# Kernel optimization log

Hardware: AMD Instinct MI355X
Metric: run time of the kernel (lower is better)

## Reference

```python
import jax, jax.numpy as jnp
import numpy as np

HEADS = 8
WS = 8  # window_size


def _relative_position_index(ws):
    coords = np.stack(np.meshgrid(np.arange(ws), np.arange(ws), indexing='ij')).reshape(2, -1)
    rel = coords[:, :, None] - coords[:, None, :]          # [2, N, N]
    rel = rel.transpose(1, 2, 0).copy()                     # [N, N, 2]
    rel[:, :, 0] += ws - 1
    rel[:, :, 1] += ws - 1
    rel[:, :, 0] *= 2 * ws - 1
    return rel.sum(-1)                                      # [N, N] int


def _window_partition(x, ws):
    B, C, H, W = x.shape
    x = x.reshape(B, C, H // ws, ws, W // ws, ws)
    x = jnp.transpose(x, (0, 2, 4, 1, 3, 5))
    return x.reshape(-1, C, ws, ws)


def _window_reverse(windows, ws, H, W):
    C = windows.shape[1]
    B = windows.shape[0] // ((H // ws) * (W // ws))
    x = windows.reshape(B, H // ws, W // ws, C, ws, ws)
    x = jnp.transpose(x, (0, 3, 1, 4, 2, 5))
    return x.reshape(B, C, H, W)


def setup_inputs() -> dict:
    key = jax.random.key(0)
    k1, k2, k3, k4 = jax.random.split(key, 4)
    B, C, H, W = 8, 256, 128, 128
    q = jax.random.normal(k1, (B, C, H, W), dtype=jnp.float32)
    k = jax.random.normal(k2, (B, C, H, W), dtype=jnp.float32)
    v = jax.random.normal(k3, (B, C, H, W), dtype=jnp.float32)
    bias_table = jax.random.normal(k4, ((2 * WS - 1) ** 2, HEADS), dtype=jnp.float32) * 0.02
    return {"q": q, "k": k, "v": v, "bias_table": bias_table, "shift_size": 4}


def reference(q, k, v, bias_table, shift_size):
    B, C, H, W = q.shape
    N = WS * WS
    hd = C // HEADS
    if shift_size > 0:
        q = jnp.roll(q, shift=(-shift_size, -shift_size), axis=(2, 3))
    qw = _window_partition(q, WS)   # [B_, C, ws, ws]
    kw = _window_partition(k, WS)
    vw = _window_partition(v, WS)
    B_ = qw.shape[0]
    # [B_, heads, hd, N] -> q,v as [B_, heads, N, hd]
    qh = jnp.transpose(qw.reshape(B_, HEADS, hd, N), (0, 1, 3, 2))
    kh = kw.reshape(B_, HEADS, hd, N)
    vh = jnp.transpose(vw.reshape(B_, HEADS, hd, N), (0, 1, 3, 2))
    scale = 1.0 / (hd ** 0.5)
    attn = jnp.einsum('bhnd,bhdm->bhnm', qh, kh) * scale
    rel_idx = _relative_position_index(WS)                  # [N, N]
    bias = bias_table[rel_idx.reshape(-1)].reshape(N, N, HEADS)
    bias = jnp.transpose(bias, (2, 0, 1))                   # [heads, N, N]
    attn = jax.nn.softmax(attn + bias[None], axis=-1)
    out = jnp.einsum('bhnm,bhmd->bhnd', attn, vh)           # [B_, heads, N, hd]
    out = jnp.transpose(out, (0, 1, 3, 2)).reshape(B_, C, WS, WS)
    x = _window_reverse(out, WS, H, W)
    if shift_size > 0:
        x = jnp.roll(x, shift=(shift_size, shift_size), axis=(2, 3))
    return x
```

## Files before the change

kernel.cpp:

```cpp
#include <hip/hip_runtime.h>


typedef __attribute__((ext_vector_type(8))) _Float16 half8;
typedef __attribute__((ext_vector_type(2))) __fp16 fp16x2;
typedef __attribute__((ext_vector_type(4))) float f32x4;
typedef unsigned int u32;

#define WSZ 8
#define HGT 128
#define WID 128
#define HWSZ (HGT * WID)
#define CCH 256
#define NHEADS 8
#define HDIM 32
#define VP 72

union __attribute__((aligned(16))) WaveBuf {
  struct { _Float16 k[32 * 72]; _Float16 q[32 * 72]; } kq;
  struct { _Float16 v[32 * VP + 8]; float o[64 * 17]; } vo;
};

__device__ __forceinline__ void lds_fence() {
  asm volatile("s_waitcnt lgkmcnt(0)" ::: "memory");
}
__device__ __forceinline__ u32 h2u(fp16x2 h) {
  union { fp16x2 h; u32 u; } c; c.h = h; return c.u;
}

__global__ void __launch_bounds__(256, 4) wattn_kernel(
    const float* __restrict__ qg, const float* __restrict__ kg,
    const float* __restrict__ vg, const float* __restrict__ btg,
    const int* __restrict__ shiftp, float* __restrict__ outg) {

  __shared__ WaveBuf wb[4];
  __shared__ float bias_lds[226];

  const int tid  = threadIdx.x;
  const int wave = tid >> 6;
  const int lane = tid & 63;
  const int quad = lane >> 4;
  const int c16  = lane & 15;

  const int bid  = blockIdx.x;
  const int wg   = bid & 3;
  const int wh   = (bid >> 2) & 15;
  const int th   = bid >> 6;
  const int head = th & (NHEADS - 1);
  const int b    = th >> 3;
  const int ww   = wg * 4 + wave;

  const int sh   = *shiftp;
  const int base = (b * CCH + head * HDIM) * HWSZ;

  f32x4 vf[8];
  {
    const float* vb = vg + base + (wh * WSZ) * WID + wg * 32;
#pragma unroll
    for (int i = 0; i < 8; ++i) {
      const int flat = i * 256 + tid;
      const int col4 = flat & 7;
      const int row  = (flat >> 3) & 7;
      const int ch   = flat >> 6;
      vf[i] = *(const f32x4*)(vb + ch * HWSZ + row * WID + col4 * 4);
    }
  }

  for (int t = tid; t < 225; t += 256)
    bias_lds[t] = btg[t * NHEADS + head] * 1.44269504088896f;

  {
    const float* kb_g = kg + base + (wh * WSZ) * WID + wg * 32;
#pragma unroll
    for (int i = 0; i < 8; ++i) {
      const int flat = i * 256 + tid;
      const int col4 = flat & 7;
      const int row  = (flat >> 3) & 7;
      const int ch   = flat >> 6;
      const f32x4 f = *(const f32x4*)(kb_g + ch * HWSZ + row * WID + col4 * 4);
      const int w  = col4 >> 1;
      const int un = (2 * row + (col4 & 1)) ^ (((ch >> 3) << 2) | (ch & 3));
      uint2 u;
      u.x = h2u(__builtin_amdgcn_cvt_pkrtz(f.x, f.y));
      u.y = h2u(__builtin_amdgcn_cvt_pkrtz(f.z, f.w));
      *(uint2*)&wb[w].kq.k[ch * 72 + un * 4] = u;
    }
  }

  if ((sh & 3) == 0) {
#pragma unroll
    for (int i = 0; i < 8; ++i) {
      const int flat = i * 256 + tid;
      const int col4 = flat & 7;
      const int row  = (flat >> 3) & 7;
      const int ch   = flat >> 6;
      const int grow = (wh * WSZ + row + sh) & (HGT - 1);
      const int gc0  = (wg * 32 + col4 * 4 + sh) & (WID - 1);
      const f32x4 f = *(const f32x4*)(qg + base + ch * HWSZ + grow * WID + gc0);
      const int w  = col4 >> 1;
      const int un = (2 * row + (col4 & 1)) ^ (((ch >> 3) << 2) | (ch & 3));
      uint2 u;
      u.x = h2u(__builtin_amdgcn_cvt_pkrtz(f.x, f.y));
      u.y = h2u(__builtin_amdgcn_cvt_pkrtz(f.z, f.w));
      *(uint2*)&wb[w].kq.q[ch * 72 + un * 4] = u;
    }
  } else {
#pragma unroll
    for (int i = 0; i < 8; ++i) {
      const int flat = i * 256 + tid;
      const int col4 = flat & 7;
      const int row  = (flat >> 3) & 7;
      const int ch   = flat >> 6;
      const int grow = (wh * WSZ + row + sh) & (HGT - 1);
      const float* qrow = qg + base + ch * HWSZ + grow * WID;
      const int cb = wg * 32 + col4 * 4 + sh;
      const float x0 = qrow[(cb + 0) & (WID - 1)];
      const float x1 = qrow[(cb + 1) & (WID - 1)];
      const float x2 = qrow[(cb + 2) & (WID - 1)];
      const float x3 = qrow[(cb + 3) & (WID - 1)];
      const int w  = col4 >> 1;
      const int un = (2 * row + (col4 & 1)) ^ (((ch >> 3) << 2) | (ch & 3));
      uint2 u;
      u.x = h2u(__builtin_amdgcn_cvt_pkrtz(x0, x1));
      u.y = h2u(__builtin_amdgcn_cvt_pkrtz(x2, x3));
      *(uint2*)&wb[w].kq.q[ch * 72 + un * 4] = u;
    }
  }

  uint2 vu[8];
#pragma unroll
  for (int i = 0; i < 8; ++i) {
    vu[i].x = h2u(__builtin_amdgcn_cvt_pkrtz(vf[i].x, vf[i].y));
    vu[i].y = h2u(__builtin_amdgcn_cvt_pkrtz(vf[i].z, vf[i].w));
  }

  __syncthreads();

  half8 aK[4], bQ[4];
  {
    const _Float16* kb = wb[wave].kq.k;
    const _Float16* qb = wb[wave].kq.q;
#pragma unroll
    for (int j = 0; j < 8; ++j) {
      const int ch = quad * 8 + j;
      const int P  = (quad << 2) | (j & 3);
      const int rb = ch * 72 + (c16 & 3);
#pragma unroll
      for (int t = 0; t < 4; ++t) {
        const int un = ((t * 4 + (c16 >> 2)) ^ P) * 4;
        aK[t][j] = kb[rb + un];
        bQ[t][j] = qb[rb + un];
      }
    }
  }

  const f32x4 zero4 = {0.f, 0.f, 0.f, 0.f};
  const float scale2 = 0.17677669529663687f * 1.44269504088896f;

  int tsub[4];
#pragma unroll
  for (int reg = 0; reg < 4; ++reg) {
    const int t = quad * 4 + reg;
    tsub[reg] = (t >> 3) * 15 + (t & 7);
  }

  u32 pk01[4][4], pk23[4][4];
  float rinv[4];

#pragma unroll
  for (int tc = 0; tc < 4; ++tc) {
    f32x4 sc[4];
#pragma unroll
    for (int tr = 0; tr < 4; ++tr)
      sc[tr] = __builtin_amdgcn_mfma_f32_16x16x32_f16(aK[tr], bQ[tc], zero4, 0, 0, 0);
    const int q64 = tc * 16 + c16;
    const int qb  = ((q64 >> 3) + 7) * 15 + (q64 & 7) + 7;
    float e[4][4], s = 0.f;
#pragma unroll
    for (int tr = 0; tr < 4; ++tr)
#pragma unroll
      for (int reg = 0; reg < 4; ++reg) {
        const float ev = __builtin_amdgcn_exp2f(
            fmaf(sc[tr][reg], scale2, bias_lds[qb - tr * 30 - tsub[reg]]));
        e[tr][reg] = ev; s += ev;
      }
    s += __shfl_xor(s, 16); s += __shfl_xor(s, 32);
    rinv[tc] = __builtin_amdgcn_rcpf(s);
#pragma unroll
    for (int tr = 0; tr < 4; ++tr) {
      pk01[tr][tc] = h2u(__builtin_amdgcn_cvt_pkrtz(e[tr][0], e[tr][1]));
      pk23[tr][tc] = h2u(__builtin_amdgcn_cvt_pkrtz(e[tr][2], e[tr][3]));
    }
  }

  __syncthreads();

  {
#pragma unroll
    for (int i = 0; i < 8; ++i) {
      const int flat = i * 256 + tid;
      const int col4 = flat & 7;
      const int row  = (flat >> 3) & 7;
      const int ch   = flat >> 6;
      const int w  = col4 >> 1;
      const int kb = row * 8 + (col4 & 1) * 4;
      *(uint2*)&wb[w].vo.v[ch * VP + kb] = vu[i];
    }
  }

  __syncthreads();

  half8 aV[2][2];
#pragma unroll
  for (int mt = 0; mt < 2; ++mt)
#pragma unroll
    for (int kc = 0; kc < 2; ++kc)
      aV[mt][kc] = *(const half8*)&wb[wave].vo.v[(mt * 16 + c16) * VP + kc * 32 + quad * 8];

  const int s0 = ((lane & 16) << 1) | c16;
  const int s1 = s0 + 16;
  const bool hi = (lane & 32) != 0;

  f32x4 of2[2][4];
#pragma unroll
  for (int mt = 0; mt < 2; ++mt)
#pragma unroll
    for (int nt = 0; nt < 4; ++nt) of2[mt][nt] = zero4;

#pragma unroll
  for (int nt = 0; nt < 4; ++nt)
#pragma unroll
    for (int kc = 0; kc < 2; ++kc) {
      const int t0 = kc * 2, t1 = kc * 2 + 1;
      const u32 w0a = __shfl(pk01[t0][nt], s0), w0b = __shfl(pk01[t1][nt], s0);
      const u32 w1a = __shfl(pk23[t0][nt], s0), w1b = __shfl(pk23[t1][nt], s0);
      const u32 w2a = __shfl(pk01[t0][nt], s1), w2b = __shfl(pk01[t1][nt], s1);
      const u32 w3a = __shfl(pk23[t0][nt], s1), w3b = __shfl(pk23[t1][nt], s1);
      union { u32 u[4]; half8 h; } bp;
      bp.u[0] = hi ? w0b : w0a;
      bp.u[1] = hi ? w1b : w1a;
      bp.u[2] = hi ? w2b : w2a;
      bp.u[3] = hi ? w3b : w3a;
#pragma unroll
      for (int mt = 0; mt < 2; ++mt)
        of2[mt][nt] = __builtin_amdgcn_mfma_f32_16x16x32_f16(aV[mt][kc], bp.h,
                                                             of2[mt][nt], 0, 0, 0);
    }

  const int hq = (wh * WSZ + (lane >> 3) + sh) & (HGT - 1);
  const int wq = (ww * WSZ + (lane & 7) + sh) & (WID - 1);
  float* ob = outg + base + hq * WID + wq;
  float* obuf = wb[wave].vo.o;

#pragma unroll
  for (int mt = 0; mt < 2; ++mt) {
    lds_fence();
#pragma unroll
    for (int nt = 0; nt < 4; ++nt)
#pragma unroll
      for (int reg = 0; reg < 4; ++reg)
        obuf[(nt * 16 + c16) * 17 + quad * 4 + reg] = of2[mt][nt][reg] * rinv[nt];
    lds_fence();
#pragma unroll
    for (int c = 0; c < 16; ++c)
      ob[(mt * 16 + c) * HWSZ] = obuf[lane * 17 + c];
  }
}

extern "C" void kernel_launch(void* const* d_in, const int* in_sizes, int n_in,
                              void* d_out, int out_size, void* d_ws, size_t ws_size,
                              hipStream_t stream) {
  const float* q  = (const float*)d_in[0];
  const float* k  = (const float*)d_in[1];
  const float* v  = (const float*)d_in[2];
  const float* bt = (const float*)d_in[3];
  const int*   sh = (const int*)d_in[4];
  float* out = (float*)d_out;

  dim3 grid(4096), block(256);
  hipLaunchKernelGGL(wattn_kernel, grid, block, 0, stream, q, k, v, bt, sh, out);
}
```

Measured before the change: 442.1 us.

## Make blocks persistent over four window groups and prefetch next K/Q

Each block now handles four consecutive column groups of windows in a loop, so the grid shrinks by four. The K and Q global loads for the next group are issued into registers before the current group's output store, so memory latency overlaps with compute and writes. Per-block bias setup is amortised across the four groups. In exchange there are fewer blocks to hide latency, more register pressure from the prefetch buffers, and an extra barrier per iteration.

```diff
diff --git a/kernel.cpp b/kernel.cpp
--- a/kernel.cpp
+++ b/kernel.cpp
@@ -27,6 +27,42 @@
   union { fp16x2 h; u32 u; } c; c.h = h; return c.u;
 }
 
+__device__ __forceinline__ void issue_kq(
+    const float* __restrict__ kg, const float* __restrict__ qg,
+    int base, int wh, int wg, int sh, int tid, f32x4* kf, f32x4* qf) {
+  const float* kb_g = kg + base + (wh * WSZ) * WID + wg * 32;
+#pragma unroll
+  for (int i = 0; i < 8; ++i) {
+    const int flat = i * 256 + tid;
+    const int col4 = flat & 7, row = (flat >> 3) & 7, ch = flat >> 6;
+    kf[i] = *(const f32x4*)(kb_g + ch * HWSZ + row * WID + col4 * 4);
+  }
+  if ((sh & 3) == 0) {
+#pragma unroll
+    for (int i = 0; i < 8; ++i) {
+      const int flat = i * 256 + tid;
+      const int col4 = flat & 7, row = (flat >> 3) & 7, ch = flat >> 6;
+      const int grow = (wh * WSZ + row + sh) & (HGT - 1);
+      const int gc0  = (wg * 32 + col4 * 4 + sh) & (WID - 1);
+      qf[i] = *(const f32x4*)(qg + base + ch * HWSZ + grow * WID + gc0);
+    }
+  } else {
+#pragma unroll
+    for (int i = 0; i < 8; ++i) {
+      const int flat = i * 256 + tid;
+      const int col4 = flat & 7, row = (flat >> 3) & 7, ch = flat >> 6;
+      const int grow = (wh * WSZ + row + sh) & (HGT - 1);
+      const float* qrow = qg + base + ch * HWSZ + grow * WID;
+      const int cb = wg * 32 + col4 * 4 + sh;
+      qf[i].x = qrow[(cb + 0) & (WID - 1)];
+      qf[i].y = qrow[(cb + 1) & (WID - 1)];
+      qf[i].z = qrow[(cb + 2) & (WID - 1)];
+      qf[i].w = qrow[(cb + 3) & (WID - 1)];
+    }
+  }
+  __builtin_amdgcn_sched_barrier(0);
+}
+
 __global__ void __launch_bounds__(256, 4) wattn_kernel(
     const float* __restrict__ qg, const float* __restrict__ kg,
     const float* __restrict__ vg, const float* __restrict__ btg,
@@ -42,119 +78,16 @@
   const int c16  = lane & 15;
 
   const int bid  = blockIdx.x;
-  const int wg   = bid & 3;
-  const int wh   = (bid >> 2) & 15;
-  const int th   = bid >> 6;
+  const int wh   = bid & 15;
+  const int th   = bid >> 4;
   const int head = th & (NHEADS - 1);
   const int b    = th >> 3;
-  const int ww   = wg * 4 + wave;
 
   const int sh   = *shiftp;
   const int base = (b * CCH + head * HDIM) * HWSZ;
 
-  f32x4 vf[8];
-  {
-    const float* vb = vg + base + (wh * WSZ) * WID + wg * 32;
-#pragma unroll
-    for (int i = 0; i < 8; ++i) {
-      const int flat = i * 256 + tid;
-      const int col4 = flat & 7;
-      const int row  = (flat >> 3) & 7;
-      const int ch   = flat >> 6;
-      vf[i] = *(const f32x4*)(vb + ch * HWSZ + row * WID + col4 * 4);
-    }
-  }
-
   for (int t = tid; t < 225; t += 256)
     bias_lds[t] = btg[t * NHEADS + head] * 1.44269504088896f;
-
-  {
-    const float* kb_g = kg + base + (wh * WSZ) * WID + wg * 32;
-#pragma unroll
-    for (int i = 0; i < 8; ++i) {
-      const int flat = i * 256 + tid;
-      const int col4 = flat & 7;
-      const int row  = (flat >> 3) & 7;
-      const int ch   = flat >> 6;
-      const f32x4 f = *(const f32x4*)(kb_g + ch * HWSZ + row * WID + col4 * 4);
-      const int w  = col4 >> 1;
-      const int un = (2 * row + (col4 & 1)) ^ (((ch >> 3) << 2) | (ch & 3));
-      uint2 u;
-      u.x = h2u(__builtin_amdgcn_cvt_pkrtz(f.x, f.y));
-      u.y = h2u(__builtin_amdgcn_cvt_pkrtz(f.z, f.w));
-      *(uint2*)&wb[w].kq.k[ch * 72 + un * 4] = u;
-    }
-  }
-
-  if ((sh & 3) == 0) {
-#pragma unroll
-    for (int i = 0; i < 8; ++i) {
-      const int flat = i * 256 + tid;
-      const int col4 = flat & 7;
-      const int row  = (flat >> 3) & 7;
-      const int ch   = flat >> 6;
-      const int grow = (wh * WSZ + row + sh) & (HGT - 1);
-      const int gc0  = (wg * 32 + col4 * 4 + sh) & (WID - 1);
-      const f32x4 f = *(const f32x4*)(qg + base + ch * HWSZ + grow * WID + gc0);
-      const int w  = col4 >> 1;
-      const int un = (2 * row + (col4 & 1)) ^ (((ch >> 3) << 2) | (ch & 3));
-      uint2 u;
-      u.x = h2u(__builtin_amdgcn_cvt_pkrtz(f.x, f.y));
-      u.y = h2u(__builtin_amdgcn_cvt_pkrtz(f.z, f.w));
-      *(uint2*)&wb[w].kq.q[ch * 72 + un * 4] = u;
-    }
-  } else {
-#pragma unroll
-    for (int i = 0; i < 8; ++i) {
-      const int flat = i * 256 + tid;
-      const int col4 = flat & 7;
-      const int row  = (flat >> 3) & 7;
-      const int ch   = flat >> 6;
-      const int grow = (wh * WSZ + row + sh) & (HGT - 1);
-      const float* qrow = qg + base + ch * HWSZ + grow * WID;
-      const int cb = wg * 32 + col4 * 4 + sh;
-      const float x0 = qrow[(cb + 0) & (WID - 1)];
-      const float x1 = qrow[(cb + 1) & (WID - 1)];
-      const float x2 = qrow[(cb + 2) & (WID - 1)];
-      const float x3 = qrow[(cb + 3) & (WID - 1)];
-      const int w  = col4 >> 1;
-      const int un = (2 * row + (col4 & 1)) ^ (((ch >> 3) << 2) | (ch & 3));
-      uint2 u;
-      u.x = h2u(__builtin_amdgcn_cvt_pkrtz(x0, x1));
-      u.y = h2u(__builtin_amdgcn_cvt_pkrtz(x2, x3));
-      *(uint2*)&wb[w].kq.q[ch * 72 + un * 4] = u;
-    }
-  }
-
-  uint2 vu[8];
-#pragma unroll
-  for (int i = 0; i < 8; ++i) {
-    vu[i].x = h2u(__builtin_amdgcn_cvt_pkrtz(vf[i].x, vf[i].y));
-    vu[i].y = h2u(__builtin_amdgcn_cvt_pkrtz(vf[i].z, vf[i].w));
-  }
-
-  __syncthreads();
-
-  half8 aK[4], bQ[4];
-  {
-    const _Float16* kb = wb[wave].kq.k;
-    const _Float16* qb = wb[wave].kq.q;
-#pragma unroll
-    for (int j = 0; j < 8; ++j) {
-      const int ch = quad * 8 + j;
-      const int P  = (quad << 2) | (j & 3);
-      const int rb = ch * 72 + (c16 & 3);
-#pragma unroll
-      for (int t = 0; t < 4; ++t) {
-        const int un = ((t * 4 + (c16 >> 2)) ^ P) * 4;
-        aK[t][j] = kb[rb + un];
-        bQ[t][j] = qb[rb + un];
-      }
-    }
-  }
-
-  const f32x4 zero4 = {0.f, 0.f, 0.f, 0.f};
-  const float scale2 = 0.17677669529663687f * 1.44269504088896f;
 
   int tsub[4];
 #pragma unroll
@@ -163,106 +96,163 @@
     tsub[reg] = (t >> 3) * 15 + (t & 7);
   }
 
-  u32 pk01[4][4], pk23[4][4];
-  float rinv[4];
-
-#pragma unroll
-  for (int tc = 0; tc < 4; ++tc) {
-    f32x4 sc[4];
-#pragma unroll
-    for (int tr = 0; tr < 4; ++tr)
-      sc[tr] = __builtin_amdgcn_mfma_f32_16x16x32_f16(aK[tr], bQ[tc], zero4, 0, 0, 0);
-    const int q64 = tc * 16 + c16;
-    const int qb  = ((q64 >> 3) + 7) * 15 + (q64 & 7) + 7;
-    float e[4][4], s = 0.f;
-#pragma unroll
-    for (int tr = 0; tr < 4; ++tr)
-#pragma unroll
-      for (int reg = 0; reg < 4; ++reg) {
-        const float ev = __builtin_amdgcn_exp2f(
-            fmaf(sc[tr][reg], scale2, bias_lds[qb - tr * 30 - tsub[reg]]));
-        e[tr][reg] = ev; s += ev;
-      }
-    s += __shfl_xor(s, 16); s += __shfl_xor(s, 32);
-    rinv[tc] = __builtin_amdgcn_rcpf(s);
-#pragma unroll
-    for (int tr = 0; tr < 4; ++tr) {
-      pk01[tr][tc] = h2u(__builtin_amdgcn_cvt_pkrtz(e[tr][0], e[tr][1]));
-      pk23[tr][tc] = h2u(__builtin_amdgcn_cvt_pkrtz(e[tr][2], e[tr][3]));
-    }
-  }
-
-  __syncthreads();
-
-  {
-#pragma unroll
-    for (int i = 0; i < 8; ++i) {
-      const int flat = i * 256 + tid;
-      const int col4 = flat & 7;
-      const int row  = (flat >> 3) & 7;
-      const int ch   = flat >> 6;
+  const f32x4 zero4 = {0.f, 0.f, 0.f, 0.f};
+  const float scale2 = 0.17677669529663687f * 1.44269504088896f;
+
+  f32x4 kf32[8], qf32[8];
+  issue_kq(kg, qg, base, wh, 0, sh, tid, kf32, qf32);
+
+  for (int it = 0; it < 4; ++it) {
+    const int wg = it;
+    const int ww = wg * 4 + wave;
+
+#pragma unroll
+    for (int i = 0; i < 8; ++i) {
+      const int flat = i * 256 + tid;
+      const int col4 = flat & 7, row = (flat >> 3) & 7, ch = flat >> 6;
+      const int w  = col4 >> 1;
+      const int un = (2 * row + (col4 & 1)) ^ (((ch >> 3) << 2) | (ch & 3));
+      uint2 uk, uq;
+      uk.x = h2u(__builtin_amdgcn_cvt_pkrtz(kf32[i].x, kf32[i].y));
+      uk.y = h2u(__builtin_amdgcn_cvt_pkrtz(kf32[i].z, kf32[i].w));
+      uq.x = h2u(__builtin_amdgcn_cvt_pkrtz(qf32[i].x, qf32[i].y));
+      uq.y = h2u(__builtin_amdgcn_cvt_pkrtz(qf32[i].z, qf32[i].w));
+      *(uint2*)&wb[w].kq.k[ch * 72 + un * 4] = uk;
+      *(uint2*)&wb[w].kq.q[ch * 72 + un * 4] = uq;
+    }
+    __syncthreads();
+
+    f32x4 vf[8];
+    {
+      const float* vb = vg + base + (wh * WSZ) * WID + wg * 32;
+#pragma unroll
+      for (int i = 0; i < 8; ++i) {
+        const int flat = i * 256 + tid;
+        const int col4 = flat & 7, row = (flat >> 3) & 7, ch = flat >> 6;
+        vf[i] = *(const f32x4*)(vb + ch * HWSZ + row * WID + col4 * 4);
+      }
+      __builtin_amdgcn_sched_barrier(0);
+    }
+
+    half8 aK[4], bQ[4];
+    {
+      const _Float16* kb = wb[wave].kq.k;
+      const _Float16* qb = wb[wave].kq.q;
+#pragma unroll
+      for (int j = 0; j < 8; ++j) {
+        const int ch = quad * 8 + j;
+        const int P  = (quad << 2) | (j & 3);
+        const int rb = ch * 72 + (c16 & 3);
+#pragma unroll
+        for (int t = 0; t < 4; ++t) {
+          const int un = ((t * 4 + (c16 >> 2)) ^ P) * 4;
+          aK[t][j] = kb[rb + un];
+          bQ[t][j] = qb[rb + un];
+        }
+      }
+    }
+
+    u32 pk01[4][4], pk23[4][4];
+    float rinv[4];
+#pragma unroll
+    for (int tc = 0; tc < 4; ++tc) {
+      f32x4 sc[4];
+#pragma unroll
+      for (int tr = 0; tr < 4; ++tr)
+        sc[tr] = __builtin_amdgcn_mfma_f32_16x16x32_f16(aK[tr], bQ[tc], zero4, 0, 0, 0);
+      const int q64 = tc * 16 + c16;
+      const int qb  = ((q64 >> 3) + 7) * 15 + (q64 & 7) + 7;
+      float e[4][4], s = 0.f;
+#pragma unroll
+      for (int tr = 0; tr < 4; ++tr)
+#pragma unroll
+        for (int reg = 0; reg < 4; ++reg) {
+          const float ev = __builtin_amdgcn_exp2f(
+              fmaf(sc[tr][reg], scale2, bias_lds[qb - tr * 30 - tsub[reg]]));
+          e[tr][reg] = ev; s += ev;
+        }
+      s += __shfl_xor(s, 16); s += __shfl_xor(s, 32);
+      rinv[tc] = __builtin_amdgcn_rcpf(s);
+#pragma unroll
+      for (int tr = 0; tr < 4; ++tr) {
+        pk01[tr][tc] = h2u(__builtin_amdgcn_cvt_pkrtz(e[tr][0], e[tr][1]));
+        pk23[tr][tc] = h2u(__builtin_amdgcn_cvt_pkrtz(e[tr][2], e[tr][3]));
+      }
+    }
+    __syncthreads();
+
+#pragma unroll
+    for (int i = 0; i < 8; ++i) {
+      const int flat = i * 256 + tid;
+      const int col4 = flat & 7, row = (flat >> 3) & 7, ch = flat >> 6;
       const int w  = col4 >> 1;
       const int kb = row * 8 + (col4 & 1) * 4;
-      *(uint2*)&wb[w].vo.v[ch * VP + kb] = vu[i];
-    }
-  }
-
-  __syncthreads();
-
-  half8 aV[2][2];
-#pragma unroll
-  for (int mt = 0; mt < 2; ++mt)
-#pragma unroll
-    for (int kc = 0; kc < 2; ++kc)
-      aV[mt][kc] = *(const half8*)&wb[wave].vo.v[(mt * 16 + c16) * VP + kc * 32 + quad * 8];
-
-  const int s0 = ((lane & 16) << 1) | c16;
-  const int s1 = s0 + 16;
-  const bool hi = (lane & 32) != 0;
-
-  f32x4 of2[2][4];
-#pragma unroll
-  for (int mt = 0; mt < 2; ++mt)
-#pragma unroll
-    for (int nt = 0; nt < 4; ++nt) of2[mt][nt] = zero4;
-
-#pragma unroll
-  for (int nt = 0; nt < 4; ++nt)
-#pragma unroll
-    for (int kc = 0; kc < 2; ++kc) {
-      const int t0 = kc * 2, t1 = kc * 2 + 1;
-      const u32 w0a = __shfl(pk01[t0][nt], s0), w0b = __shfl(pk01[t1][nt], s0);
-      const u32 w1a = __shfl(pk23[t0][nt], s0), w1b = __shfl(pk23[t1][nt], s0);
-      const u32 w2a = __shfl(pk01[t0][nt], s1), w2b = __shfl(pk01[t1][nt], s1);
-      const u32 w3a = __shfl(pk23[t0][nt], s1), w3b = __shfl(pk23[t1][nt], s1);
-      union { u32 u[4]; half8 h; } bp;
-      bp.u[0] = hi ? w0b : w0a;
-      bp.u[1] = hi ? w1b : w1a;
-      bp.u[2] = hi ? w2b : w2a;
-      bp.u[3] = hi ? w3b : w3a;
-#pragma unroll
-      for (int mt = 0; mt < 2; ++mt)
-        of2[mt][nt] = __builtin_amdgcn_mfma_f32_16x16x32_f16(aV[mt][kc], bp.h,
-                                                             of2[mt][nt], 0, 0, 0);
-    }
-
-  const int hq = (wh * WSZ + (lane >> 3) + sh) & (HGT - 1);
-  const int wq = (ww * WSZ + (lane & 7) + sh) & (WID - 1);
-  float* ob = outg + base + hq * WID + wq;
-  float* obuf = wb[wave].vo.o;
-
-#pragma unroll
-  for (int mt = 0; mt < 2; ++mt) {
-    lds_fence();
+      uint2 u;
+      u.x = h2u(__builtin_amdgcn_cvt_pkrtz(vf[i].x, vf[i].y));
+      u.y = h2u(__builtin_amdgcn_cvt_pkrtz(vf[i].z, vf[i].w));
+      *(uint2*)&wb[w].vo.v[ch * VP + kb] = u;
+    }
+    __syncthreads();
+
+    half8 aV[2][2];
+#pragma unroll
+    for (int mt = 0; mt < 2; ++mt)
+#pragma unroll
+      for (int kc = 0; kc < 2; ++kc)
+        aV[mt][kc] = *(const half8*)&wb[wave].vo.v[(mt * 16 + c16) * VP + kc * 32 + quad * 8];
+
+    const int s0 = ((lane & 16) << 1) | c16;
+    const int s1 = s0 + 16;
+    const bool hi = (lane & 32) != 0;
+
+    f32x4 of2[2][4];
+#pragma unroll
+    for (int mt = 0; mt < 2; ++mt)
+#pragma unroll
+      for (int nt = 0; nt < 4; ++nt) of2[mt][nt] = zero4;
+
 #pragma unroll
     for (int nt = 0; nt < 4; ++nt)
 #pragma unroll
-      for (int reg = 0; reg < 4; ++reg)
-        obuf[(nt * 16 + c16) * 17 + quad * 4 + reg] = of2[mt][nt][reg] * rinv[nt];
-    lds_fence();
-#pragma unroll
-    for (int c = 0; c < 16; ++c)
-      ob[(mt * 16 + c) * HWSZ] = obuf[lane * 17 + c];
+      for (int kc = 0; kc < 2; ++kc) {
+        const int t0 = kc * 2, t1 = kc * 2 + 1;
+        const u32 w0a = __shfl(pk01[t0][nt], s0), w0b = __shfl(pk01[t1][nt], s0);
+        const u32 w1a = __shfl(pk23[t0][nt], s0), w1b = __shfl(pk23[t1][nt], s0);
+        const u32 w2a = __shfl(pk01[t0][nt], s1), w2b = __shfl(pk01[t1][nt], s1);
+        const u32 w3a = __shfl(pk23[t0][nt], s1), w3b = __shfl(pk23[t1][nt], s1);
+        union { u32 u[4]; half8 h; } bp;
+        bp.u[0] = hi ? w0b : w0a;
+        bp.u[1] = hi ? w1b : w1a;
+        bp.u[2] = hi ? w2b : w2a;
+        bp.u[3] = hi ? w3b : w3a;
+#pragma unroll
+        for (int mt = 0; mt < 2; ++mt)
+          of2[mt][nt] = __builtin_amdgcn_mfma_f32_16x16x32_f16(aV[mt][kc], bp.h,
+                                                               of2[mt][nt], 0, 0, 0);
+      }
+
+    if (it < 3)
+      issue_kq(kg, qg, base, wh, wg + 1, sh, tid, kf32, qf32);
+
+    const int hq = (wh * WSZ + (lane >> 3) + sh) & (HGT - 1);
+    const int wq = (ww * WSZ + (lane & 7) + sh) & (WID - 1);
+    float* ob = outg + base + hq * WID + wq;
+    float* obuf = wb[wave].vo.o;
+
+#pragma unroll
+    for (int mt = 0; mt < 2; ++mt) {
+      lds_fence();
+#pragma unroll
+      for (int nt = 0; nt < 4; ++nt)
+#pragma unroll
+        for (int reg = 0; reg < 4; ++reg)
+          obuf[(nt * 16 + c16) * 17 + quad * 4 + reg] = of2[mt][nt][reg] * rinv[nt];
+      lds_fence();
+#pragma unroll
+      for (int c = 0; c < 16; ++c)
+        ob[(mt * 16 + c) * HWSZ] = obuf[lane * 17 + c];
+    }
+    __syncthreads();
   }
 }
 
@@ -276,6 +266,6 @@
   const int*   sh = (const int*)d_in[4];
   float* out = (float*)d_out;
 
-  dim3 grid(4096), block(256);
+  dim3 grid(1024), block(256);
   hipLaunchKernelGGL(wattn_kernel, grid, block, 0, stream, q, k, v, bt, sh, out);
 }
```

Measured after the change: 681.9 us. 54.3% more time.
